# Kernel tuning notes

Hardware: AMD Instinct MI355X
Metric: run time of the kernel (lower is better)

## Reference

```python
import jax, jax.numpy as jnp
import numpy as np

D_MODEL = 1024
N_HEADS = 16
D_HEAD = D_MODEL // N_HEADS
ROPE_BASE = 10000.0
B, L = 2, 2048


def setup_inputs() -> dict:
    key = jax.random.key(0)
    k1, k2, k3 = jax.random.split(key, 3)
    x = jax.random.normal(k1, (B, L, D_MODEL), dtype=jnp.float32)
    W_qkv = jax.random.normal(k2, (3 * D_MODEL, D_MODEL), dtype=jnp.float32) * (1.0 / np.sqrt(D_MODEL))
    W_out = jax.random.normal(k3, (D_MODEL, D_MODEL), dtype=jnp.float32) * (1.0 / np.sqrt(D_MODEL))
    position_ids = jnp.broadcast_to(jnp.arange(L, dtype=jnp.int32), (B, L))
    attn_mask_2d = jnp.broadcast_to(jnp.tril(jnp.ones((L, L), dtype=bool)), (B, L, L))
    return {"x": x, "W_qkv": W_qkv, "W_out": W_out,
            "position_ids": position_ids, "attn_mask_2d": attn_mask_2d}


def _apply_rope(t, position_ids, inv_freq):
    # t: (B, H, L, Dh) float32; position_ids: (B, L) int
    f = position_ids.astype(jnp.float32)[:, :, None] * inv_freq  # (B, L, Dh/2)
    cos = jnp.cos(f)[:, None]  # (B, 1, L, Dh/2)
    sin = jnp.sin(f)[:, None]
    x1 = t[..., 0::2]
    x2 = t[..., 1::2]
    rot_even = x1 * cos - x2 * sin
    rot_odd = x1 * sin + x2 * cos
    return jnp.stack((rot_even, rot_odd), axis=-1).reshape(t.shape)


def reference(x, W_qkv, W_out, position_ids, attn_mask_2d):
    Bb, Ll, D = x.shape
    H, Dh = N_HEADS, D // N_HEADS
    inv_freq = 1.0 / (ROPE_BASE ** (jnp.arange(0, Dh, 2, dtype=jnp.float32) / Dh))  # (Dh/2,)
    qkv = jnp.einsum('bld,ed->ble', x, W_qkv).reshape(Bb, Ll, 3, H, Dh)
    qkv = jnp.transpose(qkv, (2, 0, 3, 1, 4))  # (3, B, H, L, Dh)
    q, k, v = qkv[0], qkv[1], qkv[2]
    q = _apply_rope(q.astype(jnp.float32), position_ids, inv_freq).astype(x.dtype)
    k = _apply_rope(k.astype(jnp.float32), position_ids, inv_freq).astype(x.dtype)
    scale = 1.0 / np.sqrt(Dh).astype(np.float32)
    scores = jnp.einsum('bhld,bhmd->bhlm', q, k) * scale  # (B, H, L, L)
    neg = jnp.finfo(scores.dtype).min
    scores = jnp.where(attn_mask_2d[:, None], scores, neg)
    attn = jax.nn.softmax(scores, axis=-1)
    out = jnp.einsum('bhlm,bhmd->bhld', attn, v)
    out = jnp.transpose(out, (0, 2, 1, 3)).reshape(Bb, Ll, D)
    return jnp.einsum('bld,ed->ble', out, W_out)
```

## Files before the change

### kernel.cpp

```cpp
#include <hip/hip_runtime.h>
#include <hip/hip_bf16.h>
#include <math.h>

typedef float f32x4 __attribute__((ext_vector_type(4)));
typedef __bf16 bf16x8 __attribute__((ext_vector_type(8)));

__device__ inline f32x4 mfma16(bf16x8 a, bf16x8 b, f32x4 c) {
    return __builtin_amdgcn_mfma_f32_16x16x32_bf16(a, b, c, 0, 0, 0);
}
__device__ inline unsigned short f2bf(float f) {
    union { float f; unsigned u; } v; v.f = f;
    unsigned r = v.u + 0x7fffu + ((v.u >> 16) & 1u);
    return (unsigned short)(r >> 16);
}
__device__ inline float bf2f(unsigned short b) {
    union { unsigned u; float f; } v; v.u = ((unsigned)b) << 16;
    return v.f;
}
__device__ inline unsigned pack2(float a, float b) {
    return (unsigned)f2bf(a) | ((unsigned)f2bf(b) << 16);
}
__device__ inline f32x4 vzero() { f32x4 z = {0.f, 0.f, 0.f, 0.f}; return z; }

#define GLD16(gptr, lptr)                                                            \
    __builtin_amdgcn_global_load_lds(                                                \
        (const __attribute__((address_space(1))) unsigned int*)(const void*)(gptr),  \
        (__attribute__((address_space(3))) unsigned int*)(void*)(lptr), 16, 0, 0)

__global__ __launch_bounds__(256)
void convert_xw(const float* __restrict__ x, const float* __restrict__ wqkv,
                unsigned short* __restrict__ xb, unsigned short* __restrict__ wqkvb)
{
    int i = blockIdx.x * 256 + threadIdx.x;
    const float* src; unsigned short* dst; int off;
    if (i < 524288) { src = x;    dst = xb;    off = i; }
    else            { src = wqkv; dst = wqkvb; off = i - 524288; }
    const float4* p = (const float4*)src + (size_t)off * 2;
    float4 f0 = p[0], f1 = p[1];
    uint4 o;
    o.x = pack2(f0.x, f0.y); o.y = pack2(f0.z, f0.w);
    o.z = pack2(f1.x, f1.y); o.w = pack2(f1.z, f1.w);
    ((uint4*)dst)[off] = o;
}

template<int MI, int C32, int WPB>
__global__ __launch_bounds__(256, WPB)
void gemm_bt(const unsigned short* __restrict__ A,
             const unsigned short* __restrict__ Wt,
             void* __restrict__ C_, int M, int N, int K)
{
    __shared__ __align__(16) unsigned short As[MI * 32 * 64];
    __shared__ __align__(16) unsigned short Bs[128 * 64];

    const int tid  = threadIdx.x;
    const int wave = tid >> 6;
    const int lane = tid & 63;
    const int quad = lane >> 4;
    const int c0   = lane & 15;
    const int m0 = blockIdx.y * (MI * 32);
    const int n0 = blockIdx.x * 128;
    const int wm = (wave >> 1) * (MI * 16);
    const int wn = (wave & 1) * 64;

    const int lrow   = lane >> 3;
    const int gchunk = (lane & 7) ^ lrow;
    const int goff   = gchunk * 8;

    f32x4 acc[MI][4];
#pragma unroll
    for (int i = 0; i < MI; i++)
#pragma unroll
        for (int j = 0; j < 4; j++) acc[i][j] = vzero();

    for (int k0 = 0; k0 < K; k0 += 64) {
        __syncthreads();
#pragma unroll
        for (int p = 0; p < MI; p++) {
            int r0 = p * 32 + wave * 8;
            GLD16(&A[(size_t)(m0 + r0 + lrow) * K + k0 + goff], &As[r0 * 64]);
        }
#pragma unroll
        for (int p = 0; p < 4; p++) {
            int r0 = p * 32 + wave * 8;
            GLD16(&Wt[(size_t)(n0 + r0 + lrow) * K + k0 + goff], &Bs[r0 * 64]);
        }
        __syncthreads();
#pragma unroll
        for (int kk = 0; kk < 2; kk++) {
            const int pos = ((kk * 4 + quad) ^ (c0 & 7)) * 8;
            bf16x8 af[MI], bfr[4];
#pragma unroll
            for (int i = 0; i < MI; i++)
                af[i] = *(const bf16x8*)&As[(wm + i * 16 + c0) * 64 + pos];
#pragma unroll
            for (int j = 0; j < 4; j++)
                bfr[j] = *(const bf16x8*)&Bs[(wn + j * 16 + c0) * 64 + pos];
#pragma unroll
            for (int i = 0; i < MI; i++)
#pragma unroll
                for (int j = 0; j < 4; j++)
                    acc[i][j] = mfma16(af[i], bfr[j], acc[i][j]);
        }
    }

#pragma unroll
    for (int i = 0; i < MI; i++)
#pragma unroll
        for (int j = 0; j < 4; j++)
#pragma unroll
            for (int r = 0; r < 4; r++) {
                int row  = m0 + wm + i * 16 + quad * 4 + r;
                int colg = n0 + wn + j * 16 + c0;
                if (C32) ((float*)C_)[(size_t)row * N + colg] = acc[i][j][r];
                else ((unsigned short*)C_)[(size_t)row * N + colg] = f2bf(acc[i][j][r]);
            }
}

__global__ __launch_bounds__(256)
void rope_vtrans(const unsigned short* __restrict__ qkv,
                 const int* __restrict__ pos,
                 unsigned short* __restrict__ Qb,
                 unsigned short* __restrict__ Kb,
                 unsigned short* __restrict__ Vt,
                 const float* __restrict__ wout,
                 unsigned short* __restrict__ woutb)
{
    __shared__ unsigned short T[256 * 64];
    const int id = blockIdx.x;
    if (id < 8192) {
        int tid = id * 256 + threadIdx.x;
        int d2 = tid & 31;
        int h  = (tid >> 5) & 15;
        int l  = (tid >> 9) & 2047;
        int b  = tid >> 20;
        size_t row = (size_t)(b * 2048 + l) * 3072;
        int col = h * 64 + 2 * d2;
        float inv_freq = exp2f((float)(-2 * d2) * (13.287712379549449f / 64.0f));
        float f = (float)pos[b * 2048 + l] * inv_freq;
        float s, c;
        sincosf(f, &s, &c);
        unsigned qw = *(const unsigned*)&qkv[row + col];
        unsigned kw = *(const unsigned*)&qkv[row + 1024 + col];
        float q1 = bf2f((unsigned short)qw), q2 = bf2f((unsigned short)(qw >> 16));
        float k1 = bf2f((unsigned short)kw), k2 = bf2f((unsigned short)(kw >> 16));
        const float qs = 0.18033688011112042f;
        size_t o = ((size_t)((b * 16 + h) * 2048 + l)) * 64 + 2 * d2;
        *(unsigned*)&Qb[o] = pack2((q1 * c - q2 * s) * qs, (q1 * s + q2 * c) * qs);
        *(unsigned*)&Kb[o] = pack2(k1 * c - k2 * s, k1 * s + k2 * c);
    } else if (id < 8448) {
        const int id2 = id - 8192;
        const int t = threadIdx.x;
        const int l0 = (id2 & 7) * 256, h = (id2 >> 3) & 15, b = id2 >> 7;
#pragma unroll
        for (int i = 0; i < 8; i++) {
            int c = t + i * 256;
            int r = c >> 3, c8 = c & 7;
            int p = (c8 + (r >> 3)) & 7;
            *(uint4*)&T[r * 64 + p * 8] =
                *(const uint4*)&qkv[(size_t)(b * 2048 + l0 + r) * 3072 + 2048 + h * 64 + c8 * 8];
        }
        __syncthreads();
#pragma unroll
        for (int i = 0; i < 8; i++) {
            int c = t + i * 256;
            int dh = c >> 5, lc = c & 31;
            int blk = dh >> 3;
            unsigned short tmp[8];
#pragma unroll
            for (int j = 0; j < 8; j++) {
                int l = lc * 8 + j;
                int p = (blk + lc) & 7;
                tmp[j] = T[l * 64 + p * 8 + (dh & 7)];
            }
            *(uint4*)&Vt[((size_t)(b * 16 + h) * 64 + dh) * 2048 + l0 + lc * 8] = *(uint4*)tmp;
        }
    } else {
        int i = (id - 8448) * 256 + threadIdx.x;
        const float4* p = (const float4*)wout + (size_t)i * 2;
        float4 f0 = p[0], f1 = p[1];
        uint4 o;
        o.x = pack2(f0.x, f0.y); o.y = pack2(f0.z, f0.w);
        o.z = pack2(f1.x, f1.y); o.w = pack2(f1.z, f1.w);
        ((uint4*)woutb)[i] = o;
    }
}

__global__ __launch_bounds__(256, 2)
void attn(const unsigned short* __restrict__ Q,
          const unsigned short* __restrict__ Kb,
          const unsigned short* __restrict__ Vt,
          unsigned short* __restrict__ O)
{
    __shared__ unsigned short QsA[64 * 64];
    __shared__ unsigned short QsB[64 * 64];
    __shared__ unsigned short Ks[64 * 64];
    __shared__ unsigned short Vts[64 * 64];
    __shared__ unsigned short PsA[64 * 64];
    __shared__ unsigned short PsB[64 * 64];

    const int tid  = threadIdx.x;
    const int wave = tid >> 6;
    const int lane = tid & 63;
    const int quad = lane >> 4;
    const int c0   = lane & 15;
    const int id = blockIdx.x;
    const int jp = id >> 5;
    const int h  = id & 15;
    const int b  = (id >> 4) & 1;
    const int qtA = jp, qtB = 31 - jp;
    const size_t headoff = ((size_t)(b * 16 + h)) * 2048 * 64;
    const int q0A = qtA * 64, q0B = qtB * 64;
    const float C = 11.541560327111707f;

    const int ca = tid, cb2 = tid + 256;
    const int ra = ca >> 3, c8a = ca & 7;
    const int rb = cb2 >> 3, c8b = cb2 & 7;
    const int la = ra * 64 + (c8a ^ (ra & 7)) * 8;
    const int lb = rb * 64 + (c8b ^ (rb & 7)) * 8;

    bf16x8 ones;
#pragma unroll
    for (int j = 0; j < 8; j++) ones[j] = (__bf16)1.0f;

    uint4 kreg0, kreg1, vreg0, vreg1;
    {
        kreg0 = *(const uint4*)&Kb[headoff + (size_t)ra * 64 + c8a * 8];
        kreg1 = *(const uint4*)&Kb[headoff + (size_t)rb * 64 + c8b * 8];
        vreg0 = *(const uint4*)&Vt[headoff + (size_t)ra * 2048 + c8a * 8];
        vreg1 = *(const uint4*)&Vt[headoff + (size_t)rb * 2048 + c8b * 8];
    }
    *(uint4*)&QsA[la] = *(const uint4*)&Q[headoff + (size_t)(q0A + ra) * 64 + c8a * 8];
    *(uint4*)&QsA[lb] = *(const uint4*)&Q[headoff + (size_t)(q0A + rb) * 64 + c8b * 8];
    *(uint4*)&QsB[la] = *(const uint4*)&Q[headoff + (size_t)(q0B + ra) * 64 + c8a * 8];
    *(uint4*)&QsB[lb] = *(const uint4*)&Q[headoff + (size_t)(q0B + rb) * 64 + c8b * 8];

    f32x4 oA[4], oB[4];
#pragma unroll
    for (int j = 0; j < 4; j++) { oA[j] = vzero(); oB[j] = vzero(); }
    f32x4 laccA = vzero(), laccB = vzero();

    for (int kt = 0; kt <= qtB; kt++) {
        __syncthreads();
        *(uint4*)&Ks[la] = kreg0;
        *(uint4*)&Ks[lb] = kreg1;
        *(uint4*)&Vts[la] = vreg0;
        *(uint4*)&Vts[lb] = vreg1;
        __syncthreads();
        if (kt < qtB) {
            size_t k1o = headoff + (size_t)(kt + 1) * 4096;
            kreg0 = *(const uint4*)&Kb[k1o + (size_t)ra * 64 + c8a * 8];
            kreg1 = *(const uint4*)&Kb[k1o + (size_t)rb * 64 + c8b * 8];
            vreg0 = *(const uint4*)&Vt[headoff + (size_t)ra * 2048 + (kt + 1) * 64 + c8a * 8];
            vreg1 = *(const uint4*)&Vt[headoff + (size_t)rb * 2048 + (kt + 1) * 64 + c8b * 8];
        }
        const bool doA = (kt <= qtA);

        {
            f32x4 s[4];
#pragma unroll
            for (int nj = 0; nj < 4; nj++) s[nj] = vzero();
#pragma unroll
            for (int kk = 0; kk < 2; kk++) {
                const int pos = ((kk * 4 + quad) ^ (c0 & 7)) * 8;
                bf16x8 aq = *(const bf16x8*)&QsB[(wave * 16 + c0) * 64 + pos];
#pragma unroll
                for (int nj = 0; nj < 4; nj++) {
                    bf16x8 bk = *(const bf16x8*)&Ks[(nj * 16 + c0) * 64 + pos];
                    s[nj] = mfma16(aq, bk, s[nj]);
                }
            }
            if (kt == qtB) {
#pragma unroll
                for (int nj = 0; nj < 4; nj++)
#pragma unroll
                    for (int r = 0; r < 4; r++) {
                        int key  = nj * 16 + c0;
                        int qrow = wave * 16 + quad * 4 + r;
                        if (key > qrow) s[nj][r] = -1e38f;
                    }
            }
#pragma unroll
            for (int nj = 0; nj < 4; nj++)
#pragma unroll
                for (int r = 0; r < 4; r++) {
                    union { float f; unsigned u; } pv;
                    pv.f = __builtin_amdgcn_exp2f(s[nj][r] - C);
                    int row = wave * 16 + quad * 4 + r;
                    int col = nj * 16 + c0;
                    int pp = ((col >> 3) + row) & 7;
                    PsB[row * 64 + pp * 8 + (col & 7)] = (unsigned short)(pv.u >> 16);
                }
        }
        if (doA) {
            f32x4 s[4];
#pragma unroll
            for (int nj = 0; nj < 4; nj++) s[nj] = vzero();
#pragma unroll
            for (int kk = 0; kk < 2; kk++) {
                const int pos = ((kk * 4 + quad) ^ (c0 & 7)) * 8;
                bf16x8 aq = *(const bf16x8*)&QsA[(wave * 16 + c0) * 64 + pos];
#pragma unroll
                for (int nj = 0; nj < 4; nj++) {
                    bf16x8 bk = *(const bf16x8*)&Ks[(nj * 16 + c0) * 64 + pos];
                    s[nj] = mfma16(aq, bk, s[nj]);
                }
            }
            if (kt == qtA) {
#pragma unroll
                for (int nj = 0; nj < 4; nj++)
#pragma unroll
                    for (int r = 0; r < 4; r++) {
                        int key  = nj * 16 + c0;
                        int qrow = wave * 16 + quad * 4 + r;
                        if (key > qrow) s[nj][r] = -1e38f;
                    }
            }
#pragma unroll
            for (int nj = 0; nj < 4; nj++)
#pragma unroll
                for (int r = 0; r < 4; r++) {
                    union { float f; unsigned u; } pv;
                    pv.f = __builtin_amdgcn_exp2f(s[nj][r] - C);
                    int row = wave * 16 + quad * 4 + r;
                    int col = nj * 16 + c0;
                    int pp = ((col >> 3) + row) & 7;
                    PsA[row * 64 + pp * 8 + (col & 7)] = (unsigned short)(pv.u >> 16);
                }
        }
        asm volatile("s_waitcnt lgkmcnt(0)" ::: "memory");

#pragma unroll
        for (int kk = 0; kk < 2; kk++) {
            const int pos = ((kk * 4 + quad) ^ (c0 & 7)) * 8;
            int prow = wave * 16 + c0;
            int pp = ((kk * 4 + quad) + prow) & 7;
            bf16x8 ap = *(const bf16x8*)&PsB[prow * 64 + pp * 8];
            laccB = mfma16(ap, ones, laccB);
#pragma unroll
            for (int cj = 0; cj < 4; cj++) {
                bf16x8 bv = *(const bf16x8*)&Vts[(cj * 16 + c0) * 64 + pos];
                oB[cj] = mfma16(ap, bv, oB[cj]);
            }
        }
        if (doA) {
#pragma unroll
            for (int kk = 0; kk < 2; kk++) {
                const int pos = ((kk * 4 + quad) ^ (c0 & 7)) * 8;
                int prow = wave * 16 + c0;
                int pp = ((kk * 4 + quad) + prow) & 7;
                bf16x8 ap = *(const bf16x8*)&PsA[prow * 64 + pp * 8];
                laccA = mfma16(ap, ones, laccA);
#pragma unroll
                for (int cj = 0; cj < 4; cj++) {
                    bf16x8 bv = *(const bf16x8*)&Vts[(cj * 16 + c0) * 64 + pos];
                    oA[cj] = mfma16(ap, bv, oA[cj]);
                }
            }
        }
    }

#pragma unroll
    for (int r = 0; r < 4; r++) {
        float invA = 1.0f / laccA[r];
        float invB = 1.0f / laccB[r];
        int qlA = q0A + wave * 16 + quad * 4 + r;
        int qlB = q0B + wave * 16 + quad * 4 + r;
        size_t baseA = ((size_t)b * 2048 + qlA) * 1024 + h * 64;
        size_t baseB = ((size_t)b * 2048 + qlB) * 1024 + h * 64;
#pragma unroll
        for (int cj = 0; cj < 4; cj++) {
            O[baseA + cj * 16 + c0] = f2bf(oA[cj][r] * invA);
            O[baseB + cj * 16 + c0] = f2bf(oB[cj][r] * invB);
        }
    }
}

extern "C" void kernel_launch(void* const* d_in, const int* in_sizes, int n_in,
                              void* d_out, int out_size, void* d_ws, size_t ws_size,
                              hipStream_t stream) {
    const int* pos = (const int*)d_in[3];

    unsigned short* regA = (unsigned short*)d_ws;
    unsigned short* regB = regA + (size_t)4096 * 1024;
    unsigned short* regC = regB + (size_t)4096 * 1024;
    unsigned short* regD = regC + (size_t)4096 * 1024;
    unsigned short* regE = regD + (size_t)4096 * 3072;

    unsigned short* xb    = regA;
    unsigned short* wqkvb = regB;
    unsigned short* qkv   = regD;
    unsigned short* Qb    = regA;
    unsigned short* Kb    = regB;
    unsigned short* Vt    = regC;
    unsigned short* Ob    = regD;
    unsigned short* woutb = regE;

    convert_xw<<<3584, 256, 0, stream>>>((const float*)d_in[0], (const float*)d_in[1],
                                         xb, wqkvb);
    gemm_bt<4, 0, 4><<<dim3(24, 32), 256, 0, stream>>>(xb, wqkvb, qkv, 4096, 3072, 1024);
    rope_vtrans<<<8960, 256, 0, stream>>>(qkv, pos, Qb, Kb, Vt,
                                          (const float*)d_in[2], woutb);
    attn<<<512, 256, 0, stream>>>(Qb, Kb, Vt, Ob);
    gemm_bt<2, 1, 3><<<dim3(8, 64), 256, 0, stream>>>(Ob, woutb, d_out, 4096, 1024, 1024);
}
```

Measured before the change: 197.4 us.

## Split paired causal attention blocks into one query tile per block

Each attention block now handles one 64-row query tile instead of a balanced pair (j, 31-j), doubling the grid to 1024 blocks. Tiles are dispatched in an interleaved long/short order so the heaviest tiles start first. LDS usage halves and launch bounds rise to 4 blocks per SM, aiming for higher occupancy and better latency hiding. The cost is that K/V tiles are no longer shared between two query tiles, so K/V global and LDS traffic per unit of work roughly doubles.

```diff
diff --git a/kernel.cpp b/kernel.cpp
--- a/kernel.cpp
+++ b/kernel.cpp
@@ -185,18 +185,16 @@
     }
 }
 
-__global__ __launch_bounds__(256, 2)
+__global__ __launch_bounds__(256, 4)
 void attn(const unsigned short* __restrict__ Q,
           const unsigned short* __restrict__ Kb,
           const unsigned short* __restrict__ Vt,
           unsigned short* __restrict__ O)
 {
-    __shared__ unsigned short QsA[64 * 64];
-    __shared__ unsigned short QsB[64 * 64];
+    __shared__ unsigned short Qs[64 * 64];
     __shared__ unsigned short Ks[64 * 64];
     __shared__ unsigned short Vts[64 * 64];
-    __shared__ unsigned short PsA[64 * 64];
-    __shared__ unsigned short PsB[64 * 64];
+    __shared__ unsigned short Ps[64 * 64];
 
     const int tid  = threadIdx.x;
     const int wave = tid >> 6;
@@ -204,12 +202,15 @@
     const int quad = lane >> 4;
     const int c0   = lane & 15;
     const int id = blockIdx.x;
-    const int jp = id >> 5;
+    const int g  = id >> 5;
+    const int gg = g & 7;
+    const int gq = g >> 3;
+    const int qt = (gq == 0) ? (31 - gg) : (gq == 1) ? gg
+                 : (gq == 2) ? (23 - gg) : (8 + gg);
     const int h  = id & 15;
     const int b  = (id >> 4) & 1;
-    const int qtA = jp, qtB = 31 - jp;
     const size_t headoff = ((size_t)(b * 16 + h)) * 2048 * 64;
-    const int q0A = qtA * 64, q0B = qtB * 64;
+    const int q0 = qt * 64;
     const float C = 11.541560327111707f;
 
     const int ca = tid, cb2 = tid + 256;
@@ -229,31 +230,28 @@
         vreg0 = *(const uint4*)&Vt[headoff + (size_t)ra * 2048 + c8a * 8];
         vreg1 = *(const uint4*)&Vt[headoff + (size_t)rb * 2048 + c8b * 8];
     }
-    *(uint4*)&QsA[la] = *(const uint4*)&Q[headoff + (size_t)(q0A + ra) * 64 + c8a * 8];
-    *(uint4*)&QsA[lb] = *(const uint4*)&Q[headoff + (size_t)(q0A + rb) * 64 + c8b * 8];
-    *(uint4*)&QsB[la] = *(const uint4*)&Q[headoff + (size_t)(q0B + ra) * 64 + c8a * 8];
-    *(uint4*)&QsB[lb] = *(const uint4*)&Q[headoff + (size_t)(q0B + rb) * 64 + c8b * 8];
-
-    f32x4 oA[4], oB[4];
-#pragma unroll
-    for (int j = 0; j < 4; j++) { oA[j] = vzero(); oB[j] = vzero(); }
-    f32x4 laccA = vzero(), laccB = vzero();
-
-    for (int kt = 0; kt <= qtB; kt++) {
+    *(uint4*)&Qs[la] = *(const uint4*)&Q[headoff + (size_t)(q0 + ra) * 64 + c8a * 8];
+    *(uint4*)&Qs[lb] = *(const uint4*)&Q[headoff + (size_t)(q0 + rb) * 64 + c8b * 8];
+
+    f32x4 o[4];
+#pragma unroll
+    for (int j = 0; j < 4; j++) o[j] = vzero();
+    f32x4 lacc = vzero();
+
+    for (int kt = 0; kt <= qt; kt++) {
         __syncthreads();
         *(uint4*)&Ks[la] = kreg0;
         *(uint4*)&Ks[lb] = kreg1;
         *(uint4*)&Vts[la] = vreg0;
         *(uint4*)&Vts[lb] = vreg1;
         __syncthreads();
-        if (kt < qtB) {
+        if (kt < qt) {
             size_t k1o = headoff + (size_t)(kt + 1) * 4096;
             kreg0 = *(const uint4*)&Kb[k1o + (size_t)ra * 64 + c8a * 8];
             kreg1 = *(const uint4*)&Kb[k1o + (size_t)rb * 64 + c8b * 8];
             vreg0 = *(const uint4*)&Vt[headoff + (size_t)ra * 2048 + (kt + 1) * 64 + c8a * 8];
             vreg1 = *(const uint4*)&Vt[headoff + (size_t)rb * 2048 + (kt + 1) * 64 + c8b * 8];
         }
-        const bool doA = (kt <= qtA);
 
         {
             f32x4 s[4];
@@ -262,14 +260,14 @@
 #pragma unroll
             for (int kk = 0; kk < 2; kk++) {
                 const int pos = ((kk * 4 + quad) ^ (c0 & 7)) * 8;
-                bf16x8 aq = *(const bf16x8*)&QsB[(wave * 16 + c0) * 64 + pos];
+                bf16x8 aq = *(const bf16x8*)&Qs[(wave * 16 + c0) * 64 + pos];
 #pragma unroll
                 for (int nj = 0; nj < 4; nj++) {
                     bf16x8 bk = *(const bf16x8*)&Ks[(nj * 16 + c0) * 64 + pos];
                     s[nj] = mfma16(aq, bk, s[nj]);
                 }
             }
-            if (kt == qtB) {
+            if (kt == qt) {
 #pragma unroll
                 for (int nj = 0; nj < 4; nj++)
 #pragma unroll
@@ -288,43 +286,7 @@
                     int row = wave * 16 + quad * 4 + r;
                     int col = nj * 16 + c0;
                     int pp = ((col >> 3) + row) & 7;
-                    PsB[row * 64 + pp * 8 + (col & 7)] = (unsigned short)(pv.u >> 16);
-                }
-        }
-        if (doA) {
-            f32x4 s[4];
-#pragma unroll
-            for (int nj = 0; nj < 4; nj++) s[nj] = vzero();
-#pragma unroll
-            for (int kk = 0; kk < 2; kk++) {
-                const int pos = ((kk * 4 + quad) ^ (c0 & 7)) * 8;
-                bf16x8 aq = *(const bf16x8*)&QsA[(wave * 16 + c0) * 64 + pos];
-#pragma unroll
-                for (int nj = 0; nj < 4; nj++) {
-                    bf16x8 bk = *(const bf16x8*)&Ks[(nj * 16 + c0) * 64 + pos];
-                    s[nj] = mfma16(aq, bk, s[nj]);
-                }
-            }
-            if (kt == qtA) {
-#pragma unroll
-                for (int nj = 0; nj < 4; nj++)
-#pragma unroll
-                    for (int r = 0; r < 4; r++) {
-                        int key  = nj * 16 + c0;
-                        int qrow = wave * 16 + quad * 4 + r;
-                        if (key > qrow) s[nj][r] = -1e38f;
-                    }
-            }
-#pragma unroll
-            for (int nj = 0; nj < 4; nj++)
-#pragma unroll
-                for (int r = 0; r < 4; r++) {
-                    union { float f; unsigned u; } pv;
-                    pv.f = __builtin_amdgcn_exp2f(s[nj][r] - C);
-                    int row = wave * 16 + quad * 4 + r;
-                    int col = nj * 16 + c0;
-                    int pp = ((col >> 3) + row) & 7;
-                    PsA[row * 64 + pp * 8 + (col & 7)] = (unsigned short)(pv.u >> 16);
+                    Ps[row * 64 + pp * 8 + (col & 7)] = (unsigned short)(pv.u >> 16);
                 }
         }
         asm volatile("s_waitcnt lgkmcnt(0)" ::: "memory");
@@ -334,43 +296,24 @@
             const int pos = ((kk * 4 + quad) ^ (c0 & 7)) * 8;
             int prow = wave * 16 + c0;
             int pp = ((kk * 4 + quad) + prow) & 7;
-            bf16x8 ap = *(const bf16x8*)&PsB[prow * 64 + pp * 8];
-            laccB = mfma16(ap, ones, laccB);
+            bf16x8 ap = *(const bf16x8*)&Ps[prow * 64 + pp * 8];
+            lacc = mfma16(ap, ones, lacc);
 #pragma unroll
             for (int cj = 0; cj < 4; cj++) {
                 bf16x8 bv = *(const bf16x8*)&Vts[(cj * 16 + c0) * 64 + pos];
-                oB[cj] = mfma16(ap, bv, oB[cj]);
-            }
-        }
-        if (doA) {
-#pragma unroll
-            for (int kk = 0; kk < 2; kk++) {
-                const int pos = ((kk * 4 + quad) ^ (c0 & 7)) * 8;
-                int prow = wave * 16 + c0;
-                int pp = ((kk * 4 + quad) + prow) & 7;
-                bf16x8 ap = *(const bf16x8*)&PsA[prow * 64 + pp * 8];
-                laccA = mfma16(ap, ones, laccA);
-#pragma unroll
-                for (int cj = 0; cj < 4; cj++) {
-                    bf16x8 bv = *(const bf16x8*)&Vts[(cj * 16 + c0) * 64 + pos];
-                    oA[cj] = mfma16(ap, bv, oA[cj]);
-                }
+                o[cj] = mfma16(ap, bv, o[cj]);
             }
         }
     }
 
 #pragma unroll
     for (int r = 0; r < 4; r++) {
-        float invA = 1.0f / laccA[r];
-        float invB = 1.0f / laccB[r];
-        int qlA = q0A + wave * 16 + quad * 4 + r;
-        int qlB = q0B + wave * 16 + quad * 4 + r;
-        size_t baseA = ((size_t)b * 2048 + qlA) * 1024 + h * 64;
-        size_t baseB = ((size_t)b * 2048 + qlB) * 1024 + h * 64;
+        float inv = 1.0f / lacc[r];
+        int ql = q0 + wave * 16 + quad * 4 + r;
+        size_t base = ((size_t)b * 2048 + ql) * 1024 + h * 64;
 #pragma unroll
         for (int cj = 0; cj < 4; cj++) {
-            O[baseA + cj * 16 + c0] = f2bf(oA[cj][r] * invA);
-            O[baseB + cj * 16 + c0] = f2bf(oB[cj][r] * invB);
+            O[base + cj * 16 + c0] = f2bf(o[cj][r] * inv);
         }
     }
 }
@@ -400,6 +343,6 @@
     gemm_bt<4, 0, 4><<<dim3(24, 32), 256, 0, stream>>>(xb, wqkvb, qkv, 4096, 3072, 1024);
     rope_vtrans<<<8960, 256, 0, stream>>>(qkv, pos, Qb, Kb, Vt,
                                           (const float*)d_in[2], woutb);
-    attn<<<512, 256, 0, stream>>>(Qb, Kb, Vt, Ob);
+    attn<<<1024, 256, 0, stream>>>(Qb, Kb, Vt, Ob);
     gemm_bt<2, 1, 3><<<dim3(8, 64), 256, 0, stream>>>(Ob, woutb, d_out, 4096, 1024, 1024);
 }
```

New measurement: 201.6 us. +2.1%, slower.

## Process two KV tiles per barrier pair, keep Q in registers, add MFMA priority

Applied to the files above, without the earlier changes.

The attention loop now stages two 64-key K/V tiles into shared memory per iteration, which halves the number of __syncthreads pairs. The register prefetch covers two tiles ahead. Q fragments are loaded straight from global memory into registers, removing the QsA/QsB shared buffers and their LDS reads. s_setprio is raised around the MFMA sections so that waves issuing matrix work are favoured. The cost is higher register pressure from the extra prefetch registers and the resident Q fragments, which could lower occupancy under launch_bounds(256,2).

```diff
diff --git a/kernel.cpp b/kernel.cpp
--- a/kernel.cpp
+++ b/kernel.cpp
@@ -191,10 +191,8 @@
           const unsigned short* __restrict__ Vt,
           unsigned short* __restrict__ O)
 {
-    __shared__ unsigned short QsA[64 * 64];
-    __shared__ unsigned short QsB[64 * 64];
-    __shared__ unsigned short Ks[64 * 64];
-    __shared__ unsigned short Vts[64 * 64];
+    __shared__ unsigned short Ks2[2][64 * 64];
+    __shared__ unsigned short Vts2[2][64 * 64];
     __shared__ unsigned short PsA[64 * 64];
     __shared__ unsigned short PsB[64 * 64];
 
@@ -222,54 +220,46 @@
 #pragma unroll
     for (int j = 0; j < 8; j++) ones[j] = (__bf16)1.0f;
 
-    uint4 kreg0, kreg1, vreg0, vreg1;
-    {
-        kreg0 = *(const uint4*)&Kb[headoff + (size_t)ra * 64 + c8a * 8];
-        kreg1 = *(const uint4*)&Kb[headoff + (size_t)rb * 64 + c8b * 8];
-        vreg0 = *(const uint4*)&Vt[headoff + (size_t)ra * 2048 + c8a * 8];
-        vreg1 = *(const uint4*)&Vt[headoff + (size_t)rb * 2048 + c8b * 8];
-    }
-    *(uint4*)&QsA[la] = *(const uint4*)&Q[headoff + (size_t)(q0A + ra) * 64 + c8a * 8];
-    *(uint4*)&QsA[lb] = *(const uint4*)&Q[headoff + (size_t)(q0A + rb) * 64 + c8b * 8];
-    *(uint4*)&QsB[la] = *(const uint4*)&Q[headoff + (size_t)(q0B + ra) * 64 + c8a * 8];
-    *(uint4*)&QsB[lb] = *(const uint4*)&Q[headoff + (size_t)(q0B + rb) * 64 + c8b * 8];
+    const size_t qbaseA = headoff + (size_t)(q0A + wave * 16 + c0) * 64;
+    const size_t qbaseB = headoff + (size_t)(q0B + wave * 16 + c0) * 64;
+    bf16x8 aqA0 = *(const bf16x8*)&Q[qbaseA + quad * 8];
+    bf16x8 aqA1 = *(const bf16x8*)&Q[qbaseA + (4 + quad) * 8];
+    bf16x8 aqB0 = *(const bf16x8*)&Q[qbaseB + quad * 8];
+    bf16x8 aqB1 = *(const bf16x8*)&Q[qbaseB + (4 + quad) * 8];
+
+    uint4 kE0 = *(const uint4*)&Kb[headoff + (size_t)ra * 64 + c8a * 8];
+    uint4 kE1 = *(const uint4*)&Kb[headoff + (size_t)rb * 64 + c8b * 8];
+    uint4 vE0 = *(const uint4*)&Vt[headoff + (size_t)ra * 2048 + c8a * 8];
+    uint4 vE1 = *(const uint4*)&Vt[headoff + (size_t)rb * 2048 + c8b * 8];
+    uint4 kO0 = *(const uint4*)&Kb[headoff + 4096 + (size_t)ra * 64 + c8a * 8];
+    uint4 kO1 = *(const uint4*)&Kb[headoff + 4096 + (size_t)rb * 64 + c8b * 8];
+    uint4 vO0 = *(const uint4*)&Vt[headoff + (size_t)ra * 2048 + 64 + c8a * 8];
+    uint4 vO1 = *(const uint4*)&Vt[headoff + (size_t)rb * 2048 + 64 + c8b * 8];
 
     f32x4 oA[4], oB[4];
 #pragma unroll
     for (int j = 0; j < 4; j++) { oA[j] = vzero(); oB[j] = vzero(); }
     f32x4 laccA = vzero(), laccB = vzero();
 
-    for (int kt = 0; kt <= qtB; kt++) {
-        __syncthreads();
-        *(uint4*)&Ks[la] = kreg0;
-        *(uint4*)&Ks[lb] = kreg1;
-        *(uint4*)&Vts[la] = vreg0;
-        *(uint4*)&Vts[lb] = vreg1;
-        __syncthreads();
-        if (kt < qtB) {
-            size_t k1o = headoff + (size_t)(kt + 1) * 4096;
-            kreg0 = *(const uint4*)&Kb[k1o + (size_t)ra * 64 + c8a * 8];
-            kreg1 = *(const uint4*)&Kb[k1o + (size_t)rb * 64 + c8b * 8];
-            vreg0 = *(const uint4*)&Vt[headoff + (size_t)ra * 2048 + (kt + 1) * 64 + c8a * 8];
-            vreg1 = *(const uint4*)&Vt[headoff + (size_t)rb * 2048 + (kt + 1) * 64 + c8b * 8];
-        }
-        const bool doA = (kt <= qtA);
-
+    auto chunk_compute = [&](const unsigned short* KsC, const unsigned short* VtsC,
+                             int kc) {
         {
             f32x4 s[4];
 #pragma unroll
             for (int nj = 0; nj < 4; nj++) s[nj] = vzero();
+            __builtin_amdgcn_s_setprio(1);
 #pragma unroll
             for (int kk = 0; kk < 2; kk++) {
                 const int pos = ((kk * 4 + quad) ^ (c0 & 7)) * 8;
-                bf16x8 aq = *(const bf16x8*)&QsB[(wave * 16 + c0) * 64 + pos];
+                bf16x8 aq = kk ? aqB1 : aqB0;
 #pragma unroll
                 for (int nj = 0; nj < 4; nj++) {
-                    bf16x8 bk = *(const bf16x8*)&Ks[(nj * 16 + c0) * 64 + pos];
+                    bf16x8 bk = *(const bf16x8*)&KsC[(nj * 16 + c0) * 64 + pos];
                     s[nj] = mfma16(aq, bk, s[nj]);
                 }
             }
-            if (kt == qtB) {
+            __builtin_amdgcn_s_setprio(0);
+            if (kc == qtB) {
 #pragma unroll
                 for (int nj = 0; nj < 4; nj++)
 #pragma unroll
@@ -291,21 +281,23 @@
                     PsB[row * 64 + pp * 8 + (col & 7)] = (unsigned short)(pv.u >> 16);
                 }
         }
-        if (doA) {
+        if (kc <= qtA) {
             f32x4 s[4];
 #pragma unroll
             for (int nj = 0; nj < 4; nj++) s[nj] = vzero();
+            __builtin_amdgcn_s_setprio(1);
 #pragma unroll
             for (int kk = 0; kk < 2; kk++) {
                 const int pos = ((kk * 4 + quad) ^ (c0 & 7)) * 8;
-                bf16x8 aq = *(const bf16x8*)&QsA[(wave * 16 + c0) * 64 + pos];
+                bf16x8 aq = kk ? aqA1 : aqA0;
 #pragma unroll
                 for (int nj = 0; nj < 4; nj++) {
-                    bf16x8 bk = *(const bf16x8*)&Ks[(nj * 16 + c0) * 64 + pos];
+                    bf16x8 bk = *(const bf16x8*)&KsC[(nj * 16 + c0) * 64 + pos];
                     s[nj] = mfma16(aq, bk, s[nj]);
                 }
             }
-            if (kt == qtA) {
+            __builtin_amdgcn_s_setprio(0);
+            if (kc == qtA) {
 #pragma unroll
                 for (int nj = 0; nj < 4; nj++)
 #pragma unroll
@@ -329,6 +321,7 @@
         }
         asm volatile("s_waitcnt lgkmcnt(0)" ::: "memory");
 
+        __builtin_amdgcn_s_setprio(1);
 #pragma unroll
         for (int kk = 0; kk < 2; kk++) {
             const int pos = ((kk * 4 + quad) ^ (c0 & 7)) * 8;
@@ -338,11 +331,13 @@
             laccB = mfma16(ap, ones, laccB);
 #pragma unroll
             for (int cj = 0; cj < 4; cj++) {
-                bf16x8 bv = *(const bf16x8*)&Vts[(cj * 16 + c0) * 64 + pos];
+                bf16x8 bv = *(const bf16x8*)&VtsC[(cj * 16 + c0) * 64 + pos];
                 oB[cj] = mfma16(ap, bv, oB[cj]);
             }
         }
-        if (doA) {
+        __builtin_amdgcn_s_setprio(0);
+        if (kc <= qtA) {
+            __builtin_amdgcn_s_setprio(1);
 #pragma unroll
             for (int kk = 0; kk < 2; kk++) {
                 const int pos = ((kk * 4 + quad) ^ (c0 & 7)) * 8;
@@ -352,11 +347,47 @@
                 laccA = mfma16(ap, ones, laccA);
 #pragma unroll
                 for (int cj = 0; cj < 4; cj++) {
-                    bf16x8 bv = *(const bf16x8*)&Vts[(cj * 16 + c0) * 64 + pos];
+                    bf16x8 bv = *(const bf16x8*)&VtsC[(cj * 16 + c0) * 64 + pos];
                     oA[cj] = mfma16(ap, bv, oA[cj]);
                 }
             }
-        }
+            __builtin_amdgcn_s_setprio(0);
+        }
+    };
+
+    const int nkv = (qtB >> 1) + 1;
+    for (int kt2 = 0; kt2 < nkv; kt2++) {
+        const int ce = 2 * kt2, co = ce + 1;
+        const bool hasOdd = (co <= qtB);
+        __syncthreads();
+        *(uint4*)&Ks2[0][la] = kE0;
+        *(uint4*)&Ks2[0][lb] = kE1;
+        *(uint4*)&Vts2[0][la] = vE0;
+        *(uint4*)&Vts2[0][lb] = vE1;
+        if (hasOdd) {
+            *(uint4*)&Ks2[1][la] = kO0;
+            *(uint4*)&Ks2[1][lb] = kO1;
+            *(uint4*)&Vts2[1][la] = vO0;
+            *(uint4*)&Vts2[1][lb] = vO1;
+        }
+        __syncthreads();
+        if (kt2 + 1 < nkv) {
+            const int ne = ce + 2, no = ce + 3;
+            size_t k1o = headoff + (size_t)ne * 4096;
+            kE0 = *(const uint4*)&Kb[k1o + (size_t)ra * 64 + c8a * 8];
+            kE1 = *(const uint4*)&Kb[k1o + (size_t)rb * 64 + c8b * 8];
+            vE0 = *(const uint4*)&Vt[headoff + (size_t)ra * 2048 + ne * 64 + c8a * 8];
+            vE1 = *(const uint4*)&Vt[headoff + (size_t)rb * 2048 + ne * 64 + c8b * 8];
+            if (no <= qtB) {
+                size_t k2o = headoff + (size_t)no * 4096;
+                kO0 = *(const uint4*)&Kb[k2o + (size_t)ra * 64 + c8a * 8];
+                kO1 = *(const uint4*)&Kb[k2o + (size_t)rb * 64 + c8b * 8];
+                vO0 = *(const uint4*)&Vt[headoff + (size_t)ra * 2048 + no * 64 + c8a * 8];
+                vO1 = *(const uint4*)&Vt[headoff + (size_t)rb * 2048 + no * 64 + c8b * 8];
+            }
+        }
+        chunk_compute(Ks2[0], Vts2[0], ce);
+        if (hasOdd) chunk_compute(Ks2[1], Vts2[1], co);
     }
 
 #pragma unroll
```

After: 195.5 us. No clear change (-1.0%).
